# Optimization experiments

Measured on AMD Instinct MI355X. Metric: run time of the kernel, lower is better.

Reference implementation:

```python
import jax, jax.numpy as jnp
import numpy as np

B, L, N, D = 64, 12, 883, 64
T, MEM_NUM, MEM_DIM = 12, 64, 64


def setup_inputs() -> dict:
    key = jax.random.key(0)
    k1, k2 = jax.random.split(key)
    x = jax.random.normal(k1, (B, L, N, D), dtype=jnp.float32)
    # xavier_normal_ on (T, mem_num, mem_dim): fan_in=mem_dim, fan_out=mem_num (last two dims)
    std = float(np.sqrt(2.0 / (MEM_NUM + MEM_DIM)))
    M = jax.random.normal(k2, (T, MEM_NUM, MEM_DIM), dtype=jnp.float32) * std
    return {"x": x, "M": M}


def reference(x, M):
    # score[b,t,n,m] = sum_{l,d} x[b,l,n,d] * M[t,m,d]  (note: l is summed, per original einsum)
    score = jax.nn.softmax(jnp.einsum('blnd,tmd->btnm', x, M), axis=-1)
    # value[b,t,n,d] = sum_m score[b,t,n,m] * M[t,m,d]
    value = jnp.einsum('btnm,tmd->btnd', score, M)
    return value
```

## Files before the change

kernel.cpp:

```cpp
#include <hip/hip_runtime.h>
#include <hip/hip_bf16.h>

#define B_ 64
#define L_ 12
#define N_ 883
#define D_ 64
#define T_ 12
#define M_ 64
#define NTILES 14
#define NHALF 7

typedef __bf16 bf16x8 __attribute__((ext_vector_type(8)));
typedef __bf16 bf16x4 __attribute__((ext_vector_type(4)));
typedef float  f32x4  __attribute__((ext_vector_type(4)));

__global__ __launch_bounds__(256) void prep_all(const float* __restrict__ x,
                                                const float* __restrict__ M,
                                                __bf16* __restrict__ Mh,
                                                __bf16* __restrict__ Ml,
                                                __bf16* __restrict__ Mth,
                                                __bf16* __restrict__ xs_hi,
                                                __bf16* __restrict__ xs_lo) {
    const size_t XS_F4 = (size_t)B_ * N_ * 16;
    size_t idx = (size_t)blockIdx.x * 256 + threadIdx.x;
    if (idx < XS_F4) {
        size_t b   = idx / (N_ * 16);
        size_t rem = idx - b * (N_ * 16);
        const f32x4* xp = (const f32x4*)x + b * (size_t)(L_ * N_ * 16) + rem;
        f32x4 s = f32x4{0.f, 0.f, 0.f, 0.f};
        #pragma unroll
        for (int l = 0; l < L_; ++l)
            s += xp[(size_t)l * (N_ * 16)];
        bf16x4 h4, l4;
        #pragma unroll
        for (int i = 0; i < 4; ++i) {
            __bf16 h = (__bf16)s[i];
            h4[i] = h;
            l4[i] = (__bf16)(s[i] - (float)h);
        }
        ((bf16x4*)xs_hi)[idx] = h4;
        ((bf16x4*)xs_lo)[idx] = l4;
    } else {
        size_t j = idx - XS_F4;
        if (j < (size_t)T_ * M_ * D_) {
            float v = M[j];
            __bf16 h = (__bf16)v;
            __bf16 l = (__bf16)(v - (float)h);
            Mh[j] = h;
            Ml[j] = l;
            int t = (int)(j >> 12);
            int m = (int)(j >> 6) & 63;
            int d = (int)j & 63;
            Mth[(t << 12) + (d << 6) + m] = h;
        }
    }
}

__global__ __launch_bounds__(256, 2) void fused_attn(
        const __bf16* __restrict__ xs_hi,
        const __bf16* __restrict__ xs_lo,
        const __bf16* __restrict__ Mh,
        const __bf16* __restrict__ Ml,
        const __bf16* __restrict__ Mth,
        float* __restrict__ out) {
    __shared__ __bf16 pbf[4][16][72];

    const int tid  = threadIdx.x;
    const int lane = tid & 63;
    const int wave = tid >> 6;
    const int l15  = lane & 15;
    const int quad = lane >> 4;

    const int nh = blockIdx.x;
    const int t  = blockIdx.y;
    const int b  = blockIdx.z;

    const __bf16* mh  = Mh  + (t << 12);
    const __bf16* ml  = Ml  + (t << 12);
    const __bf16* mth = Mth + (t << 12);

    bf16x8 bmh[4][2], bml[4][2], bmv[4][2];
    #pragma unroll
    for (int mt = 0; mt < 4; ++mt) {
        #pragma unroll
        for (int kc = 0; kc < 2; ++kc) {
            const size_t off = (size_t)(mt * 16 + l15) * 64 + kc * 32 + quad * 8;
            bmh[mt][kc] = *(const bf16x8*)(mh + off);
            bml[mt][kc] = *(const bf16x8*)(ml + off);
            bmv[mt][kc] = *(const bf16x8*)(mth + off);
        }
    }

    const __bf16* xhb = xs_hi + (size_t)b * N_ * D_;
    const __bf16* xlb = xs_lo + (size_t)b * N_ * D_;
    float* outb = out + ((size_t)(b * T_ + t) * N_) * D_;

    bf16x8 a_h[2][2], a_l[2][2];

    {
        const int n0   = nh * NHALF * 64;
        const int arow = n0 + wave * 16 + l15;
        const int arc  = arow < N_ ? arow : (N_ - 1);
        #pragma unroll
        for (int kc = 0; kc < 2; ++kc) {
            a_h[0][kc] = *(const bf16x8*)(xhb + (size_t)arc * D_ + kc * 32 + quad * 8);
            a_l[0][kc] = *(const bf16x8*)(xlb + (size_t)arc * D_ + kc * 32 + quad * 8);
        }
    }

    #pragma unroll
    for (int i = 0; i < NHALF; ++i) {
        const int cur = i & 1;
        const int n0  = (nh * NHALF + i) * 64;

        if (i + 1 < NHALF) {
            const int arow = n0 + 64 + wave * 16 + l15;
            const int arc  = arow < N_ ? arow : (N_ - 1);
            #pragma unroll
            for (int kc = 0; kc < 2; ++kc) {
                a_h[cur ^ 1][kc] = *(const bf16x8*)(xhb + (size_t)arc * D_ + kc * 32 + quad * 8);
                a_l[cur ^ 1][kc] = *(const bf16x8*)(xlb + (size_t)arc * D_ + kc * 32 + quad * 8);
            }
        }

        f32x4 c1[4];
        #pragma unroll
        for (int mt = 0; mt < 4; ++mt) c1[mt] = f32x4{0.f, 0.f, 0.f, 0.f};
        #pragma unroll
        for (int mt = 0; mt < 4; ++mt) {
            #pragma unroll
            for (int kc = 0; kc < 2; ++kc) {
                c1[mt] = __builtin_amdgcn_mfma_f32_16x16x32_bf16(a_h[cur][kc], bmh[mt][kc], c1[mt], 0, 0, 0);
                c1[mt] = __builtin_amdgcn_mfma_f32_16x16x32_bf16(a_l[cur][kc], bmh[mt][kc], c1[mt], 0, 0, 0);
                c1[mt] = __builtin_amdgcn_mfma_f32_16x16x32_bf16(a_h[cur][kc], bml[mt][kc], c1[mt], 0, 0, 0);
            }
        }

        #pragma unroll
        for (int r = 0; r < 4; ++r) {
            float mx = fmaxf(fmaxf(c1[0][r], c1[1][r]), fmaxf(c1[2][r], c1[3][r]));
            #pragma unroll
            for (int off = 1; off < 16; off <<= 1)
                mx = fmaxf(mx, __shfl_xor(mx, off));
            float e[4];
            float s = 0.f;
            #pragma unroll
            for (int mt = 0; mt < 4; ++mt) {
                e[mt] = __expf(c1[mt][r] - mx);
                s += e[mt];
            }
            #pragma unroll
            for (int off = 1; off < 16; off <<= 1)
                s += __shfl_xor(s, off);
            float inv = 1.0f / s;
            #pragma unroll
            for (int mt = 0; mt < 4; ++mt)
                pbf[wave][quad * 4 + r][mt * 16 + l15] = (__bf16)(e[mt] * inv);
        }

        bf16x8 pa[2];
        #pragma unroll
        for (int kc = 0; kc < 2; ++kc)
            pa[kc] = *(const bf16x8*)&pbf[wave][l15][kc * 32 + quad * 8];

        f32x4 c2[4];
        #pragma unroll
        for (int dt = 0; dt < 4; ++dt) c2[dt] = f32x4{0.f, 0.f, 0.f, 0.f};
        #pragma unroll
        for (int dt = 0; dt < 4; ++dt) {
            #pragma unroll
            for (int kc = 0; kc < 2; ++kc)
                c2[dt] = __builtin_amdgcn_mfma_f32_16x16x32_bf16(pa[kc], bmv[dt][kc], c2[dt], 0, 0, 0);
        }

        float* op = outb + (size_t)n0 * D_;
        #pragma unroll
        for (int dt = 0; dt < 4; ++dt) {
            #pragma unroll
            for (int r = 0; r < 4; ++r) {
                int row = wave * 16 + quad * 4 + r;
                if (n0 + row < N_)
                    op[(size_t)row * D_ + dt * 16 + l15] = c2[dt][r];
            }
        }
    }
}

extern "C" void kernel_launch(void* const* d_in, const int* in_sizes, int n_in,
                              void* d_out, int out_size, void* d_ws, size_t ws_size,
                              hipStream_t stream) {
    const float* x = (const float*)d_in[0];
    const float* M = (const float*)d_in[1];
    float* out = (float*)d_out;

    __bf16* Mh    = (__bf16*)d_ws;
    __bf16* Ml    = Mh + T_ * M_ * D_;
    __bf16* Mth   = Ml + T_ * M_ * D_;
    __bf16* xs_hi = Mth + T_ * M_ * D_;
    __bf16* xs_lo = xs_hi + (size_t)B_ * N_ * D_;

    const int xs_blocks   = (B_ * N_ * 16) / 256;
    const int prep_blocks = (T_ * M_ * D_ + 255) / 256;
    prep_all<<<xs_blocks + prep_blocks, 256, 0, stream>>>(x, M, Mh, Ml, Mth, xs_hi, xs_lo);

    fused_attn<<<dim3(2, T_, B_), 256, 0, stream>>>(xs_hi, xs_lo, Mh, Ml, Mth, out);
}
```

Measured before the change: 329.4 us.

## Stage M in shared memory, raise occupancy, and defer softmax normalization

The attention kernel now loads the per-t M tiles (hi, lo and transposed) into shared memory once per block, instead of holding 24 bf16x8 fragments per thread in registers. This frees registers so launch bounds can request 4 blocks per CU instead of 2. The softmax drops the max-subtraction pass and normalizes the output after the PV MFMA, which shortens the dependency chain and removes one shuffle reduction. Without the max subtraction, larger score magnitudes could overflow exp. The prep kernel issues all L loads before a tree reduction to expose more memory-level parallelism.

```diff
diff --git a/kernel.cpp b/kernel.cpp
--- a/kernel.cpp
+++ b/kernel.cpp
@@ -7,7 +7,6 @@
 #define D_ 64
 #define T_ 12
 #define M_ 64
-#define NTILES 14
 #define NHALF 7
 
 typedef __bf16 bf16x8 __attribute__((ext_vector_type(8)));
@@ -27,10 +26,14 @@
         size_t b   = idx / (N_ * 16);
         size_t rem = idx - b * (N_ * 16);
         const f32x4* xp = (const f32x4*)x + b * (size_t)(L_ * N_ * 16) + rem;
-        f32x4 s = f32x4{0.f, 0.f, 0.f, 0.f};
+        f32x4 v[L_];
         #pragma unroll
         for (int l = 0; l < L_; ++l)
-            s += xp[(size_t)l * (N_ * 16)];
+            v[l] = xp[(size_t)l * (N_ * 16)];
+        #pragma unroll
+        for (int l = 0; l < 6; ++l)
+            v[l] += v[l + 6];
+        f32x4 s = ((v[0] + v[1]) + (v[2] + v[3])) + (v[4] + v[5]);
         bf16x4 h4, l4;
         #pragma unroll
         for (int i = 0; i < 4; ++i) {
@@ -56,13 +59,16 @@
     }
 }
 
-__global__ __launch_bounds__(256, 2) void fused_attn(
+__global__ __launch_bounds__(256, 4) void fused_attn(
         const __bf16* __restrict__ xs_hi,
         const __bf16* __restrict__ xs_lo,
         const __bf16* __restrict__ Mh,
         const __bf16* __restrict__ Ml,
         const __bf16* __restrict__ Mth,
         float* __restrict__ out) {
+    __shared__ __bf16 mhv[64][72];
+    __shared__ __bf16 mlv[64][72];
+    __shared__ __bf16 mtv[64][72];
     __shared__ __bf16 pbf[4][16][72];
 
     const int tid  = threadIdx.x;
@@ -75,31 +81,26 @@
     const int t  = blockIdx.y;
     const int b  = blockIdx.z;
 
-    const __bf16* mh  = Mh  + (t << 12);
-    const __bf16* ml  = Ml  + (t << 12);
-    const __bf16* mth = Mth + (t << 12);
-
-    bf16x8 bmh[4][2], bml[4][2], bmv[4][2];
-    #pragma unroll
-    for (int mt = 0; mt < 4; ++mt) {
-        #pragma unroll
-        for (int kc = 0; kc < 2; ++kc) {
-            const size_t off = (size_t)(mt * 16 + l15) * 64 + kc * 32 + quad * 8;
-            bmh[mt][kc] = *(const bf16x8*)(mh + off);
-            bml[mt][kc] = *(const bf16x8*)(ml + off);
-            bmv[mt][kc] = *(const bf16x8*)(mth + off);
-        }
-    }
+    {
+        const int row = tid >> 2;
+        const int c16 = (tid & 3) * 16;
+        const size_t g = ((size_t)t << 12) + (row << 6) + c16;
+        *(bf16x8*)&mhv[row][c16]     = *(const bf16x8*)(Mh + g);
+        *(bf16x8*)&mhv[row][c16 + 8] = *(const bf16x8*)(Mh + g + 8);
+        *(bf16x8*)&mlv[row][c16]     = *(const bf16x8*)(Ml + g);
+        *(bf16x8*)&mlv[row][c16 + 8] = *(const bf16x8*)(Ml + g + 8);
+        *(bf16x8*)&mtv[row][c16]     = *(const bf16x8*)(Mth + g);
+        *(bf16x8*)&mtv[row][c16 + 8] = *(const bf16x8*)(Mth + g + 8);
+    }
+    __syncthreads();
 
     const __bf16* xhb = xs_hi + (size_t)b * N_ * D_;
     const __bf16* xlb = xs_lo + (size_t)b * N_ * D_;
     float* outb = out + ((size_t)(b * T_ + t) * N_) * D_;
 
     bf16x8 a_h[2][2], a_l[2][2];
-
     {
-        const int n0   = nh * NHALF * 64;
-        const int arow = n0 + wave * 16 + l15;
+        const int arow = nh * NHALF * 64 + wave * 16 + l15;
         const int arc  = arow < N_ ? arow : (N_ - 1);
         #pragma unroll
         for (int kc = 0; kc < 2; ++kc) {
@@ -130,32 +131,25 @@
         for (int mt = 0; mt < 4; ++mt) {
             #pragma unroll
             for (int kc = 0; kc < 2; ++kc) {
-                c1[mt] = __builtin_amdgcn_mfma_f32_16x16x32_bf16(a_h[cur][kc], bmh[mt][kc], c1[mt], 0, 0, 0);
-                c1[mt] = __builtin_amdgcn_mfma_f32_16x16x32_bf16(a_l[cur][kc], bmh[mt][kc], c1[mt], 0, 0, 0);
-                c1[mt] = __builtin_amdgcn_mfma_f32_16x16x32_bf16(a_h[cur][kc], bml[mt][kc], c1[mt], 0, 0, 0);
-            }
-        }
-
+                bf16x8 bh = *(const bf16x8*)&mhv[mt * 16 + l15][kc * 32 + quad * 8];
+                bf16x8 bl = *(const bf16x8*)&mlv[mt * 16 + l15][kc * 32 + quad * 8];
+                c1[mt] = __builtin_amdgcn_mfma_f32_16x16x32_bf16(a_h[cur][kc], bh, c1[mt], 0, 0, 0);
+                c1[mt] = __builtin_amdgcn_mfma_f32_16x16x32_bf16(a_l[cur][kc], bh, c1[mt], 0, 0, 0);
+                c1[mt] = __builtin_amdgcn_mfma_f32_16x16x32_bf16(a_h[cur][kc], bl, c1[mt], 0, 0, 0);
+            }
+        }
+
+        float sden[4];
         #pragma unroll
         for (int r = 0; r < 4; ++r) {
-            float mx = fmaxf(fmaxf(c1[0][r], c1[1][r]), fmaxf(c1[2][r], c1[3][r]));
-            #pragma unroll
-            for (int off = 1; off < 16; off <<= 1)
-                mx = fmaxf(mx, __shfl_xor(mx, off));
-            float e[4];
-            float s = 0.f;
+            float s0 = 0.f;
             #pragma unroll
             for (int mt = 0; mt < 4; ++mt) {
-                e[mt] = __expf(c1[mt][r] - mx);
-                s += e[mt];
-            }
-            #pragma unroll
-            for (int off = 1; off < 16; off <<= 1)
-                s += __shfl_xor(s, off);
-            float inv = 1.0f / s;
-            #pragma unroll
-            for (int mt = 0; mt < 4; ++mt)
-                pbf[wave][quad * 4 + r][mt * 16 + l15] = (__bf16)(e[mt] * inv);
+                float e = __expf(c1[mt][r]);
+                pbf[wave][quad * 4 + r][mt * 16 + l15] = (__bf16)e;
+                s0 += e;
+            }
+            sden[r] = s0;
         }
 
         bf16x8 pa[2];
@@ -163,15 +157,28 @@
         for (int kc = 0; kc < 2; ++kc)
             pa[kc] = *(const bf16x8*)&pbf[wave][l15][kc * 32 + quad * 8];
 
+        #pragma unroll
+        for (int r = 0; r < 4; ++r) {
+            #pragma unroll
+            for (int off = 1; off < 16; off <<= 1)
+                sden[r] += __shfl_xor(sden[r], off);
+        }
+
         f32x4 c2[4];
         #pragma unroll
         for (int dt = 0; dt < 4; ++dt) c2[dt] = f32x4{0.f, 0.f, 0.f, 0.f};
         #pragma unroll
         for (int dt = 0; dt < 4; ++dt) {
             #pragma unroll
-            for (int kc = 0; kc < 2; ++kc)
-                c2[dt] = __builtin_amdgcn_mfma_f32_16x16x32_bf16(pa[kc], bmv[dt][kc], c2[dt], 0, 0, 0);
-        }
+            for (int kc = 0; kc < 2; ++kc) {
+                bf16x8 bv = *(const bf16x8*)&mtv[dt * 16 + l15][kc * 32 + quad * 8];
+                c2[dt] = __builtin_amdgcn_mfma_f32_16x16x32_bf16(pa[kc], bv, c2[dt], 0, 0, 0);
+            }
+        }
+
+        float inv[4];
+        #pragma unroll
+        for (int r = 0; r < 4; ++r) inv[r] = 1.0f / sden[r];
 
         float* op = outb + (size_t)n0 * D_;
         #pragma unroll
@@ -180,7 +187,7 @@
             for (int r = 0; r < 4; ++r) {
                 int row = wave * 16 + quad * 4 + r;
                 if (n0 + row < N_)
-                    op[(size_t)row * D_ + dt * 16 + l15] = c2[dt][r];
+                    op[(size_t)row * D_ + dt * 16 + l15] = c2[dt][r] * inv[r];
             }
         }
     }
```

After: 321.3 us. 2.5% less time.
